# Optimization experiments

Hardware: AMD Instinct MI355X
Metric: run time of the kernel (lower is better)

The kernel has to match this reference:

```python
import jax, jax.numpy as jnp
import numpy as np

B, H, L, D = 8, 8, 2048, 512

def setup_inputs() -> dict:
    key = jax.random.key(0)
    k1, k2 = jax.random.split(key)
    x = jax.random.normal(k1, (B, H, L, D), dtype=jnp.float32)
    mask = jnp.ones((B, L), dtype=jnp.int32)  # unused by the layer's call()
    complex_weight = 0.02 * jax.random.normal(k2, (H, L, D, 2), dtype=jnp.float32)
    return {"x": x, "mask": mask, "complex_weight": complex_weight}

def reference(x, mask, complex_weight):
    # FFT over the innermost (model_size) axis, matching tf.signal.fft
    fft_x = jnp.fft.fft(x.astype(jnp.complex64), axis=-1)
    w = jax.lax.complex(complex_weight[..., 0], complex_weight[..., 1])  # (H, L, D)
    gated = w * fft_x  # broadcast over batch
    out = jnp.fft.ifft(gated, axis=-1).real.astype(jnp.float32)
    return out
```

## Files before the change

### kernel.cpp

```cpp
#include <hip/hip_runtime.h>
#include <math.h>


#define HL 16384

__device__ __forceinline__ float2 cadd(float2 a, float2 b){ return make_float2(a.x+b.x, a.y+b.y); }
__device__ __forceinline__ float2 csub(float2 a, float2 b){ return make_float2(a.x-b.x, a.y-b.y); }
__device__ __forceinline__ float2 cmul(float2 a, float2 b){ return make_float2(a.x*b.x - a.y*b.y, a.x*b.y + a.y*b.x); }

__device__ __forceinline__ float2 twiddle(float f) {
    return make_float2(__builtin_amdgcn_cosf(f), -__builtin_amdgcn_sinf(f));
}

__device__ __forceinline__ void twiddle_pows(float f, float2 w[8]) {
    w[1] = twiddle(f);
    w[2] = cmul(w[1], w[1]);
    w[3] = cmul(w[1], w[2]);
    w[4] = cmul(w[2], w[2]);
    w[5] = cmul(w[1], w[4]);
    w[6] = cmul(w[2], w[4]);
    w[7] = cmul(w[3], w[4]);
}

__device__ __forceinline__ void wave_lds_fence() {
    asm volatile("s_waitcnt lgkmcnt(0)" ::: "memory");
    __builtin_amdgcn_wave_barrier();
}

__device__ __forceinline__ void fft8(float2 x[8]) {
    const float c = 0.70710678118654752f;
    float2 u0 = cadd(x[0], x[4]);
    float2 u1 = cadd(x[1], x[5]);
    float2 u2 = cadd(x[2], x[6]);
    float2 u3 = cadd(x[3], x[7]);
    float2 v0 = csub(x[0], x[4]);
    float2 t1 = csub(x[1], x[5]);
    float2 t2 = csub(x[2], x[6]);
    float2 t3 = csub(x[3], x[7]);
    float2 v1 = make_float2(c*(t1.x + t1.y), c*(t1.y - t1.x));
    float2 v2 = make_float2(t2.y, -t2.x);
    float2 v3 = make_float2(c*(t3.y - t3.x), -c*(t3.x + t3.y));
    float2 p0 = cadd(u0, u2), p1 = cadd(u1, u3);
    float2 q0 = csub(u0, u2), q1t = csub(u1, u3);
    float2 q1 = make_float2(q1t.y, -q1t.x);
    x[0] = cadd(p0, p1);
    x[4] = csub(p0, p1);
    x[2] = cadd(q0, q1);
    x[6] = csub(q0, q1);
    float2 r0 = cadd(v0, v2), r1 = cadd(v1, v3);
    float2 s0 = csub(v0, v2), s1t = csub(v1, v3);
    float2 s1 = make_float2(s1t.y, -s1t.x);
    x[1] = cadd(r0, r1);
    x[5] = csub(r0, r1);
    x[3] = cadd(s0, s1);
    x[7] = csub(s0, s1);
}

__device__ __forceinline__ void fft512x2(float2 va[8], float2 vb[8],
                                         int role, int lane,
                                         float2* __restrict__ sa,
                                         float2* __restrict__ sb)
{
    fft8(va);
    fft8(vb);
    {
        float2 w[8];
        twiddle_pows((float)role * (1.0f/512.0f), w);
        #pragma unroll
        for (int k = 1; k < 8; ++k) {
            va[k] = cmul(va[k], w[k]);
            vb[k] = cmul(vb[k], w[k]);
        }
    }
    wave_lds_fence();
    #pragma unroll
    for (int k1 = 0; k1 < 8; ++k1) {
        sa[k1*72 + role] = va[k1];
        sb[k1*72 + role] = vb[k1];
    }
    wave_lds_fence();
    const int k1 = lane >> 3, m2 = lane & 7;
    float2 ua[8], ub[8];
    #pragma unroll
    for (int m1 = 0; m1 < 8; ++m1) {
        ua[m1] = sa[k1*72 + 8*m1 + m2];
        ub[m1] = sb[k1*72 + 8*m1 + m2];
    }
    fft8(ua);
    fft8(ub);
    {
        float2 w[8];
        twiddle_pows((float)m2 * (1.0f/64.0f), w);
        #pragma unroll
        for (int j = 1; j < 8; ++j) {
            ua[j] = cmul(ua[j], w[j]);
            ub[j] = cmul(ub[j], w[j]);
        }
    }
    wave_lds_fence();
    #pragma unroll
    for (int j1 = 0; j1 < 8; ++j1) {
        sa[k1*72 + 9*j1 + m2] = ua[j1];
        sb[k1*72 + 9*j1 + m2] = ub[j1];
    }
    wave_lds_fence();
    const int j1 = lane & 7;
    #pragma unroll
    for (int m = 0; m < 8; ++m) {
        va[m] = sa[k1*72 + 9*j1 + m];
        vb[m] = sb[k1*72 + 9*j1 + m];
    }
    fft8(va);
    fft8(vb);
}

__global__ __launch_bounds__(128, 4) void sgn_fft_r8x2(
    const float* __restrict__ x,
    const float* __restrict__ cw,
    float* __restrict__ out)
{
    __shared__ float2 sc[2][2][8*72];

    const int tid  = threadIdx.x;
    const int wid  = tid >> 6;
    const int lane = tid & 63;
    const int hl   = blockIdx.x;

    const int b4a = wid * 2;
    const int b4b = b4a + 1;
    const int r1a = (b4a       * HL + hl) * 512;
    const int r2a = ((b4a + 4) * HL + hl) * 512;
    const int r1b = (b4b       * HL + hl) * 512;
    const int r2b = ((b4b + 4) * HL + hl) * 512;

    const float2* __restrict__ cw2 = (const float2*)cw;
    const int wrow = hl * 512;

    float2* __restrict__ sa = &sc[wid][0][0];
    float2* __restrict__ sb = &sc[wid][1][0];

    float2 va[8], vb[8];
    #pragma unroll
    for (int j = 0; j < 8; ++j) {
        va[j].x = x[r1a + 64*j + lane];
        va[j].y = x[r2a + 64*j + lane];
        vb[j].x = x[r1b + 64*j + lane];
        vb[j].y = x[r2b + 64*j + lane];
    }

    fft512x2(va, vb, lane, lane, sa, sb);

    const int dsl = ((lane & 7) << 3) | (lane >> 3);
    const float hs = 0.5f / 512.0f;
    #pragma unroll
    for (int j2 = 0; j2 < 8; ++j2) {
        const int k  = dsl + 64*j2;
        const int nk = (512 - k) & 511;
        const float2 wk  = cw2[wrow + k];
        const float2 wnk = cw2[wrow + nk];
        const float2 wp  = make_float2(hs*(wk.x + wnk.x), hs*(wk.y - wnk.y));
        const float2 ga  = cmul(wp, va[j2]);
        const float2 gb  = cmul(wp, vb[j2]);
        va[j2] = make_float2(ga.x, -ga.y);
        vb[j2] = make_float2(gb.x, -gb.y);
    }

    fft512x2(va, vb, dsl, lane, sa, sb);

    #pragma unroll
    for (int j2 = 0; j2 < 8; ++j2) {
        const int k = dsl + 64*j2;
        out[r1a + k] =  va[j2].x;
        out[r2a + k] = -va[j2].y;
        out[r1b + k] =  vb[j2].x;
        out[r2b + k] = -vb[j2].y;
    }
}

extern "C" void kernel_launch(void* const* d_in, const int* in_sizes, int n_in,
                              void* d_out, int out_size, void* d_ws, size_t ws_size,
                              hipStream_t stream) {
    const float* x  = (const float*)d_in[0];
    const float* cw = (const float*)d_in[2];
    float* out = (float*)d_out;

    sgn_fft_r8x2<<<dim3(HL), dim3(128), 0, stream>>>(x, cw, out);
}
```

Measured before the change: 479.6 us.

## Persistent-style blocks with async global-to-LDS prefetch of next FFT rows

Replaces the one-block-per-(h,l) launch with 2048 blocks that each loop over 8 (h,l) rows. Each wave now does a single packed 512-point FFT instead of two. The next iteration's input rows are prefetched into LDS with global_load_lds while the current row is transformed, and the weight loads are issued before the first FFT. The goal is to hide global-memory latency in what is a latency-bound kernel. The cost is reliance on hand-tuned vmcnt waits and less independent work per wave to cover latency.

```diff
diff --git a/kernel.cpp b/kernel.cpp
--- a/kernel.cpp
+++ b/kernel.cpp
@@ -2,7 +2,9 @@
 #include <math.h>
 
 
-#define HL 16384
+#define HL    16384
+#define NBLK  2048
+#define ITERS (HL / NBLK)
 
 __device__ __forceinline__ float2 cadd(float2 a, float2 b){ return make_float2(a.x+b.x, a.y+b.y); }
 __device__ __forceinline__ float2 csub(float2 a, float2 b){ return make_float2(a.x-b.x, a.y-b.y); }
@@ -56,124 +58,128 @@
     x[7] = csub(s0, s1);
 }
 
-__device__ __forceinline__ void fft512x2(float2 va[8], float2 vb[8],
-                                         int role, int lane,
-                                         float2* __restrict__ sa,
-                                         float2* __restrict__ sb)
+__device__ __forceinline__ void fft512(float2 v[8], int role, int lane, float2* sc)
 {
-    fft8(va);
-    fft8(vb);
+    fft8(v);
     {
         float2 w[8];
         twiddle_pows((float)role * (1.0f/512.0f), w);
         #pragma unroll
-        for (int k = 1; k < 8; ++k) {
-            va[k] = cmul(va[k], w[k]);
-            vb[k] = cmul(vb[k], w[k]);
-        }
+        for (int k = 1; k < 8; ++k) v[k] = cmul(v[k], w[k]);
     }
     wave_lds_fence();
     #pragma unroll
-    for (int k1 = 0; k1 < 8; ++k1) {
-        sa[k1*72 + role] = va[k1];
-        sb[k1*72 + role] = vb[k1];
-    }
+    for (int k1 = 0; k1 < 8; ++k1) sc[k1*72 + role] = v[k1];
     wave_lds_fence();
     const int k1 = lane >> 3, m2 = lane & 7;
-    float2 ua[8], ub[8];
+    float2 u[8];
     #pragma unroll
-    for (int m1 = 0; m1 < 8; ++m1) {
-        ua[m1] = sa[k1*72 + 8*m1 + m2];
-        ub[m1] = sb[k1*72 + 8*m1 + m2];
-    }
-    fft8(ua);
-    fft8(ub);
+    for (int m1 = 0; m1 < 8; ++m1) u[m1] = sc[k1*72 + 8*m1 + m2];
+    fft8(u);
     {
         float2 w[8];
         twiddle_pows((float)m2 * (1.0f/64.0f), w);
         #pragma unroll
-        for (int j = 1; j < 8; ++j) {
-            ua[j] = cmul(ua[j], w[j]);
-            ub[j] = cmul(ub[j], w[j]);
-        }
+        for (int j = 1; j < 8; ++j) u[j] = cmul(u[j], w[j]);
     }
     wave_lds_fence();
     #pragma unroll
-    for (int j1 = 0; j1 < 8; ++j1) {
-        sa[k1*72 + 9*j1 + m2] = ua[j1];
-        sb[k1*72 + 9*j1 + m2] = ub[j1];
-    }
+    for (int j1 = 0; j1 < 8; ++j1) sc[k1*72 + 9*j1 + m2] = u[j1];
     wave_lds_fence();
     const int j1 = lane & 7;
     #pragma unroll
-    for (int m = 0; m < 8; ++m) {
-        va[m] = sa[k1*72 + 9*j1 + m];
-        vb[m] = sb[k1*72 + 9*j1 + m];
-    }
-    fft8(va);
-    fft8(vb);
+    for (int m = 0; m < 8; ++m) v[m] = sc[k1*72 + 9*j1 + m];
+    fft8(v);
 }
 
-__global__ __launch_bounds__(128, 4) void sgn_fft_r8x2(
+using gu32 = __attribute__((address_space(1))) const unsigned int;
+using lu32 = __attribute__((address_space(3))) unsigned int;
+
+__global__ __launch_bounds__(256) void sgn_fft_pipe(
     const float* __restrict__ x,
     const float* __restrict__ cw,
     float* __restrict__ out)
 {
-    __shared__ float2 sc[2][2][8*72];
+    __shared__ __align__(16) float2 sc[4][8*72];
+    __shared__ __align__(16) float  inb[4][2][512];
 
     const int tid  = threadIdx.x;
     const int wid  = tid >> 6;
     const int lane = tid & 63;
-    const int hl   = blockIdx.x;
-
-    const int b4a = wid * 2;
-    const int b4b = b4a + 1;
-    const int r1a = (b4a       * HL + hl) * 512;
-    const int r2a = ((b4a + 4) * HL + hl) * 512;
-    const int r1b = (b4b       * HL + hl) * 512;
-    const int r2b = ((b4b + 4) * HL + hl) * 512;
+    const int dsl  = ((lane & 7) << 3) | (lane >> 3);
 
     const float2* __restrict__ cw2 = (const float2*)cw;
-    const int wrow = hl * 512;
+    float2* scw = &sc[wid][0];
 
-    float2* __restrict__ sa = &sc[wid][0][0];
-    float2* __restrict__ sb = &sc[wid][1][0];
+    {
+        const int hl = blockIdx.x;
+        const int r1 = (wid       * HL + hl) * 512;
+        const int r2 = ((wid + 4) * HL + hl) * 512;
+        #pragma unroll
+        for (int c = 0; c < 2; ++c) {
+            __builtin_amdgcn_global_load_lds((gu32*)(x + r1 + c*256 + lane*4),
+                                             (lu32*)(&inb[wid][0][c*256]), 16, 0, 0);
+            __builtin_amdgcn_global_load_lds((gu32*)(x + r2 + c*256 + lane*4),
+                                             (lu32*)(&inb[wid][1][c*256]), 16, 0, 0);
+        }
+    }
+    asm volatile("s_waitcnt vmcnt(0)" ::: "memory");
 
-    float2 va[8], vb[8];
-    #pragma unroll
-    for (int j = 0; j < 8; ++j) {
-        va[j].x = x[r1a + 64*j + lane];
-        va[j].y = x[r2a + 64*j + lane];
-        vb[j].x = x[r1b + 64*j + lane];
-        vb[j].y = x[r2b + 64*j + lane];
-    }
+    #pragma unroll 1
+    for (int it = 0; it < ITERS; ++it) {
+        const int hl = blockIdx.x + NBLK * it;
+        const int r1 = (wid       * HL + hl) * 512;
+        const int r2 = ((wid + 4) * HL + hl) * 512;
+        const int wrow = hl * 512;
 
-    fft512x2(va, vb, lane, lane, sa, sb);
+        asm volatile("s_waitcnt vmcnt(16)" ::: "memory");
 
-    const int dsl = ((lane & 7) << 3) | (lane >> 3);
-    const float hs = 0.5f / 512.0f;
-    #pragma unroll
-    for (int j2 = 0; j2 < 8; ++j2) {
-        const int k  = dsl + 64*j2;
-        const int nk = (512 - k) & 511;
-        const float2 wk  = cw2[wrow + k];
-        const float2 wnk = cw2[wrow + nk];
-        const float2 wp  = make_float2(hs*(wk.x + wnk.x), hs*(wk.y - wnk.y));
-        const float2 ga  = cmul(wp, va[j2]);
-        const float2 gb  = cmul(wp, vb[j2]);
-        va[j2] = make_float2(ga.x, -ga.y);
-        vb[j2] = make_float2(gb.x, -gb.y);
-    }
+        float2 v[8];
+        #pragma unroll
+        for (int j = 0; j < 8; ++j) {
+            v[j].x = inb[wid][0][64*j + lane];
+            v[j].y = inb[wid][1][64*j + lane];
+        }
+        wave_lds_fence();
 
-    fft512x2(va, vb, dsl, lane, sa, sb);
+        if (it + 1 < ITERS) {
+            const int hln = hl + NBLK;
+            const int r1n = (wid       * HL + hln) * 512;
+            const int r2n = ((wid + 4) * HL + hln) * 512;
+            #pragma unroll
+            for (int c = 0; c < 2; ++c) {
+                __builtin_amdgcn_global_load_lds((gu32*)(x + r1n + c*256 + lane*4),
+                                                 (lu32*)(&inb[wid][0][c*256]), 16, 0, 0);
+                __builtin_amdgcn_global_load_lds((gu32*)(x + r2n + c*256 + lane*4),
+                                                 (lu32*)(&inb[wid][1][c*256]), 16, 0, 0);
+            }
+        }
 
-    #pragma unroll
-    for (int j2 = 0; j2 < 8; ++j2) {
-        const int k = dsl + 64*j2;
-        out[r1a + k] =  va[j2].x;
-        out[r2a + k] = -va[j2].y;
-        out[r1b + k] =  vb[j2].x;
-        out[r2b + k] = -vb[j2].y;
+        float2 wk[8];
+        #pragma unroll
+        for (int j2 = 0; j2 < 8; ++j2) wk[j2] = cw2[wrow + dsl + 64*j2];
+
+        fft512(v, lane, lane, scw);
+
+        const float hs = 0.5f / 512.0f;
+        #pragma unroll
+        for (int j2 = 0; j2 < 8; ++j2) {
+            const int k  = dsl + 64*j2;
+            const int nk = (512 - k) & 511;
+            const float2 wnk = cw2[wrow + nk];
+            const float2 wp  = make_float2(hs*(wk[j2].x + wnk.x), hs*(wk[j2].y - wnk.y));
+            const float2 g   = cmul(wp, v[j2]);
+            v[j2] = make_float2(g.x, -g.y);
+        }
+
+        fft512(v, dsl, lane, scw);
+
+        #pragma unroll
+        for (int j2 = 0; j2 < 8; ++j2) {
+            const int k = dsl + 64*j2;
+            out[r1 + k] =  v[j2].x;
+            out[r2 + k] = -v[j2].y;
+        }
     }
 }
 
@@ -184,5 +190,5 @@
     const float* cw = (const float*)d_in[2];
     float* out = (float*)d_out;
 
-    sgn_fft_r8x2<<<dim3(HL), dim3(128), 0, stream>>>(x, cw, out);
+    sgn_fft_pipe<<<dim3(NBLK), dim3(256), 0, stream>>>(x, cw, out);
 }
```

Result: no change. 485.1 us (+1.1%).
